# Kernel tuning notes

Hardware: AMD Instinct MI355X
Metric: run time of the kernel (lower is better)

## Reference

```python
import jax, jax.numpy as jnp
import numpy as np

D_MODEL = 1024
NUM_HEADS = 16


def setup_inputs() -> dict:
    key = jax.random.key(0)
    ks = jax.random.split(key, 11)
    B, S, D = 2, 2048, D_MODEL
    s = 1.0 / np.sqrt(D)
    return {
        "queries": jax.random.normal(ks[0], (B, S, D), jnp.float32),
        "keys": jax.random.normal(ks[1], (B, S, D), jnp.float32),
        "values": jax.random.normal(ks[2], (B, S, D), jnp.float32),
        "W_q": jax.random.normal(ks[3], (D, D), jnp.float32) * s,
        "b_q": jnp.zeros((D,), jnp.float32),
        "W_k": jax.random.normal(ks[4], (D, D), jnp.float32) * s,
        "b_k": jnp.zeros((D,), jnp.float32),
        "W_v": jax.random.normal(ks[5], (D, D), jnp.float32) * s,
        "b_v": jnp.zeros((D,), jnp.float32),
        "W_o": jax.random.normal(ks[6], (D, D), jnp.float32) * s,
        "b_o": jnp.zeros((D,), jnp.float32),
    }


def _split_heads(x, num_heads):
    # [B, S, D] -> [B, H, S, d_h]
    B, S, D = x.shape
    return x.reshape(B, S, num_heads, D // num_heads).transpose(0, 2, 1, 3)


def reference(queries, keys, values, W_q, b_q, W_k, b_k, W_v, b_v, W_o, b_o):
    H = NUM_HEADS
    Q = _split_heads(queries @ W_q.T + b_q, H)  # [B,H,S,dh]
    K = _split_heads(keys @ W_k.T + b_k, H)
    V = _split_heads(values @ W_v.T + b_v, H)
    d = Q.shape[-1]
    scores = jnp.einsum("bhqd,bhkd->bhqk", Q, K) / jnp.sqrt(jnp.asarray(d, Q.dtype))
    attn = jax.nn.softmax(scores, axis=-1)
    out = jnp.einsum("bhqk,bhkd->bhqd", attn, V)  # [B,H,S,dh]
    B, _, S, _ = out.shape
    out = out.transpose(0, 2, 1, 3).reshape(B, S, -1)  # combine heads
    return out @ W_o.T + b_o
```

## Files before the change

### kernel.cpp

```cpp
#include <hip/hip_runtime.h>
#include <cstdint>
#include <cmath>

typedef short s16x8 __attribute__((ext_vector_type(8)));
typedef short s16x4 __attribute__((ext_vector_type(4)));
typedef float f32x4 __attribute__((ext_vector_type(4)));
typedef unsigned int u32;

#define AS_G __attribute__((address_space(1)))
#define AS_L __attribute__((address_space(3)))

#define QSCALE 0.18033688011112042f

__device__ __forceinline__ void ld16_to_lds(const void* g, const void* l) {
    __builtin_amdgcn_global_load_lds((AS_G void*)(g), (AS_L void*)(l), 16, 0, 0);
}

__device__ __forceinline__ short f2bf(float f) {
    union { float f; uint32_t u; } v; v.f = f;
    uint32_t r = v.u + 0x7fffu + ((v.u >> 16) & 1u);
    return (short)(r >> 16);
}

template<int F32OUT, int NJ, int QKV>
__global__ __launch_bounds__(256, 3)
void gemm_bt(const short* __restrict__ Abase, long Az,
             const short* __restrict__ Wbase, long Wz,
             const float* __restrict__ bias0, const float* __restrict__ bias1,
             const float* __restrict__ bias2,
             void* __restrict__ Obase, long Oz,
             const int M, const int N, const int K)
{
    constexpr int BN = NJ * 32;
    constexpr int BSt = (BN * 4) / 256;
    constexpr int LPS = 2 + BSt;
    __shared__ __align__(16) short As[3][128 * 32];
    __shared__ __align__(16) short Bs[3][BN * 32];

    const int t = threadIdx.x, lane = t & 63, wv = t >> 6;
    const int wr = wv >> 1, wc = wv & 1;
    const int q4 = lane >> 4, l16 = lane & 15;

    const u32 gx = gridDim.x, gy = gridDim.y;
    u32 lin = blockIdx.x + gx * (blockIdx.y + gy * blockIdx.z);
    const u32 nwg = gx * gy * gridDim.z;
    if ((nwg & 7u) == 0u) lin = (lin & 7u) * (nwg >> 3) + (lin >> 3);
    const int bxs = lin % gx;
    const u32 rem = lin / gx;
    const int bys = rem % gy;
    const int z   = rem / gy;

    const short* A  = Abase + (long)z * Az;
    const short* Bt = Wbase + (long)z * Wz;
    const float* bias = (z == 0) ? bias0 : ((z == 1) ? bias1 : bias2);
    const float bmul = (QKV && z == 0) ? QSCALE : 1.0f;
    const int bn0 = bxs * BN, bm0 = bys * 128;

    f32x4 acc[4][NJ] = {};

    const short* gA[2];
    const short* gB[BSt];
    #pragma unroll
    for (int s = 0; s < 2; ++s) {
        const int c = t + 256 * s;
        const int r = c >> 2, g = (c & 3) ^ ((c >> 3) & 3);
        gA[s] = A + (size_t)(bm0 + r) * K + g * 8;
    }
    #pragma unroll
    for (int s = 0; s < BSt; ++s) {
        const int c = t + 256 * s;
        const int r = c >> 2, g = (c & 3) ^ ((c >> 3) & 3);
        gB[s] = Bt + (size_t)(bn0 + r) * K + g * 8;
    }

    auto stage = [&](int buf) {
        #pragma unroll
        for (int s = 0; s < 2; ++s) {
            ld16_to_lds(gA[s], &As[buf][(wv * 64 + 256 * s) * 8]);
            gA[s] += 32;
        }
        #pragma unroll
        for (int s = 0; s < BSt; ++s) {
            ld16_to_lds(gB[s], &Bs[buf][(wv * 64 + 256 * s) * 8]);
            gB[s] += 32;
        }
    };

    const int kIters = K >> 5;
    stage(0);
    stage(1);
    for (int kt = 0; kt < kIters; ++kt) {
        const int cur = kt % 3;
        if (kt < kIters - 1)
            asm volatile("s_waitcnt vmcnt(%0)" :: "n"(LPS) : "memory");
        else
            asm volatile("s_waitcnt vmcnt(0)" ::: "memory");
        __builtin_amdgcn_s_barrier();
        __builtin_amdgcn_sched_barrier(0);
        if (kt + 2 < kIters) stage((kt + 2) % 3);

        s16x8 aF[4], bF[NJ];
        #pragma unroll
        for (int i = 0; i < 4; ++i) {
            const int m = wr * 64 + i * 16 + l16;
            aF[i] = *(const s16x8*)&As[cur][m * 32 + (q4 ^ ((m >> 1) & 3)) * 8];
        }
        #pragma unroll
        for (int j = 0; j < NJ; ++j) {
            const int n = wc * (BN / 2) + j * 16 + l16;
            bF[j] = *(const s16x8*)&Bs[cur][n * 32 + (q4 ^ ((n >> 1) & 3)) * 8];
        }
        #pragma unroll
        for (int i = 0; i < 4; ++i)
            #pragma unroll
            for (int j = 0; j < NJ; ++j)
                acc[i][j] = __builtin_amdgcn_mfma_f32_16x16x32_bf16(
                    aF[i], bF[j], acc[i][j], 0, 0, 0);
    }

    #pragma unroll
    for (int j = 0; j < NJ; ++j) {
        const int col = bn0 + wc * (BN / 2) + j * 16 + l16;
        const float bj = bias[col] * bmul;
        #pragma unroll
        for (int i = 0; i < 4; ++i) {
            const int row0 = bm0 + wr * 64 + i * 16 + q4 * 4;
            if (QKV && z == 2) {
                s16x4 ov;
                #pragma unroll
                for (int r = 0; r < 4; ++r) ov[r] = f2bf(acc[i][j][r] + bj);
                *(s16x4*)(((short*)Obase + (long)z * Oz) +
                          (size_t)col * 4096 + row0) = ov;
            } else {
                #pragma unroll
                for (int r = 0; r < 4; ++r) {
                    const float v = acc[i][j][r] + bj;
                    if (F32OUT)
                        ((float*)Obase + (long)z * Oz)[(size_t)(row0 + r) * N + col] = v;
                    else
                        ((short*)Obase + (long)z * Oz)[(size_t)(row0 + r) * N + col] = f2bf(v);
                }
            }
        }
    }
}

__global__ __launch_bounds__(256, 4)
void attn_fwd(const short* __restrict__ Qp, const short* __restrict__ Kp,
              const short* __restrict__ VpT, short* __restrict__ Out)
{
    constexpr int D = 1024, S = 2048;
    __shared__ __align__(16) short Ks[2][512 * 8];
    __shared__ __align__(16) short Vt[2][512 * 8];

    const int t = threadIdx.x, lane = t & 63, wv = t >> 6;
    const int q4 = lane >> 4, l16 = lane & 15;
    const int bid = blockIdx.x;
    const int qt = (bid >> 3) & 31;
    const int hb = (bid & 7) * 4 + (bid >> 8);
    const int h = hb >> 1, b = hb & 1;
    const size_t rowB = (size_t)b * S;
    const int cb = h * 64;
    const int qrow0 = qt * 64 + wv * 16;

    s16x8 qF[2];
    #pragma unroll
    for (int tk = 0; tk < 2; ++tk)
        qF[tk] = *(const s16x8*)
            &Qp[(rowB + qrow0 + l16) * D + cb + tk * 32 + q4 * 8];

    f32x4 oacc[4] = {};
    f32x4 lacc = {};
    s16x8 onesF;
    #pragma unroll
    for (int e = 0; e < 8; ++e) onesF[e] = (short)0x3F80;

    const short* KpB = Kp + rowB * D + cb;
    const short* VtG = VpT + (size_t)cb * 4096 + b * 2048;

    auto stageKV = [&](int buf, int kv0) {
        #pragma unroll
        for (int s = 0; s < 2; ++s) {
            const int slot = (4 * s + wv) * 64 + lane;
            const int r = slot >> 3;
            const int kcs = (slot & 7) ^ (r & 7);
            ld16_to_lds(KpB + (size_t)(kv0 + r) * D + kcs * 8,
                        &Ks[buf][(wv * 64 + 256 * s) * 8]);
        }
        #pragma unroll
        for (int s = 0; s < 2; ++s) {
            const int c = t + 256 * s;
            const int d = c >> 3, kcp = c & 7;
            ld16_to_lds(VtG + (size_t)d * 4096 + kv0 + ((kcp ^ (d & 7)) * 8),
                        &Vt[buf][(wv * 64 + 256 * s) * 8]);
        }
    };

    stageKV(0, 0);

    for (int kvt = 0; kvt < 32; ++kvt) {
        const int kv0 = kvt * 64;
        __syncthreads();
        if (kvt < 31) stageKV((kvt + 1) & 1, kv0 + 64);

        f32x4 acc[4] = {};
        #pragma unroll
        for (int tk = 0; tk < 2; ++tk) {
            s16x8 kA[4];
            #pragma unroll
            for (int j = 0; j < 4; ++j)
                kA[j] = *(const s16x8*)
                    &Ks[kvt & 1][((j * 16 + l16) * 8 +
                                  ((tk * 4 + q4) ^ (l16 & 7))) * 8];
            #pragma unroll
            for (int j = 0; j < 4; ++j)
                acc[j] = __builtin_amdgcn_mfma_f32_16x16x32_bf16(
                    kA[j], qF[tk], acc[j], 0, 0, 0);
        }

        u32 c[4][2];
        #pragma unroll
        for (int j = 0; j < 4; ++j) {
            const float p0 = __builtin_amdgcn_exp2f(acc[j][0]);
            const float p1 = __builtin_amdgcn_exp2f(acc[j][1]);
            const float p2 = __builtin_amdgcn_exp2f(acc[j][2]);
            const float p3 = __builtin_amdgcn_exp2f(acc[j][3]);
            asm("v_cvt_pk_bf16_f32 %0, %1, %2" : "=v"(c[j][0]) : "v"(p0), "v"(p1));
            asm("v_cvt_pk_bf16_f32 %0, %1, %2" : "=v"(c[j][1]) : "v"(p2), "v"(p3));
        }

        union { s16x8 v; u32 w[4]; } pA[2];
        #pragma unroll
        for (int tkp = 0; tkp < 2; ++tkp) {
            #pragma unroll
            for (int bb = 0; bb < 2; ++bb) {
                u32 x = c[2 * tkp][bb], y = c[2 * tkp + 1][bb];
                asm("v_permlane32_swap_b32 %0, %1" : "+v"(x), "+v"(y));
                asm("v_permlane16_swap_b32 %0, %1" : "+v"(x), "+v"(y));
                pA[tkp].w[bb] = x;
                pA[tkp].w[2 + bb] = y;
            }
        }

        #pragma unroll
        for (int tkp = 0; tkp < 2; ++tkp) {
            lacc = __builtin_amdgcn_mfma_f32_16x16x32_bf16(
                pA[tkp].v, onesF, lacc, 0, 0, 0);
            #pragma unroll
            for (int jd = 0; jd < 4; ++jd) {
                const int d = jd * 16 + l16;
                const s16x8 vF = *(const s16x8*)
                    &Vt[kvt & 1][(d * 8 + ((tkp * 4 + q4) ^ (d & 7))) * 8];
                oacc[jd] = __builtin_amdgcn_mfma_f32_16x16x32_bf16(
                    pA[tkp].v, vF, oacc[jd], 0, 0, 0);
            }
        }
    }

    #pragma unroll
    for (int r = 0; r < 4; ++r) {
        const float inv = 1.0f / lacc[r];
        const size_t row = rowB + qrow0 + q4 * 4 + r;
        #pragma unroll
        for (int jd = 0; jd < 4; ++jd)
            Out[row * D + cb + jd * 16 + l16] = f2bf(oacc[jd][r] * inv);
    }
}

__global__ __launch_bounds__(256)
void cast_all(const float* __restrict__ q, const float* __restrict__ k,
              const float* __restrict__ v, const float* __restrict__ wq,
              const float* __restrict__ wk, const float* __restrict__ wv,
              const float* __restrict__ wo, short* __restrict__ out)
{
    const size_t i = ((size_t)blockIdx.x * 256 + threadIdx.x) * 8;
    const float* src; size_t off;
    if      (i < 4194304)  { src = q;  off = i; }
    else if (i < 8388608)  { src = k;  off = i - 4194304; }
    else if (i < 12582912) { src = v;  off = i - 8388608; }
    else if (i < 13631488) { src = wq; off = i - 12582912; }
    else if (i < 14680064) { src = wk; off = i - 13631488; }
    else if (i < 15728640) { src = wv; off = i - 14680064; }
    else                   { src = wo; off = i - 15728640; }
    const float m = (i >= 12582912 && i < 13631488) ? QSCALE : 1.0f;
    const float4 a = *(const float4*)(src + off);
    const float4 c = *(const float4*)(src + off + 4);
    s16x8 o;
    o[0] = f2bf(a.x * m); o[1] = f2bf(a.y * m); o[2] = f2bf(a.z * m); o[3] = f2bf(a.w * m);
    o[4] = f2bf(c.x * m); o[5] = f2bf(c.y * m); o[6] = f2bf(c.z * m); o[7] = f2bf(c.w * m);
    *(s16x8*)(out + i) = o;
}

extern "C" void kernel_launch(void* const* d_in, const int* in_sizes, int n_in,
                              void* d_out, int out_size, void* d_ws, size_t ws_size,
                              hipStream_t stream)
{
    const float* q  = (const float*)d_in[0];
    const float* k  = (const float*)d_in[1];
    const float* v  = (const float*)d_in[2];
    const float* Wq = (const float*)d_in[3];
    const float* bq = (const float*)d_in[4];
    const float* Wk = (const float*)d_in[5];
    const float* bk = (const float*)d_in[6];
    const float* Wv = (const float*)d_in[7];
    const float* bv = (const float*)d_in[8];
    const float* Wo = (const float*)d_in[9];
    const float* bo = (const float*)d_in[10];

    short* ws = (short*)d_ws;
    const long MEL = 1048576;
    short* Aq  = ws;
    short* Wqb = ws + 12 * MEL;
    short* Wob = ws + 15 * MEL;
    short* Qp  = ws + 16 * MEL;
    short* Kp  = ws + 20 * MEL;
    short* VpT = ws + 24 * MEL;
    short* AO  = ws;

    cast_all<<<8192, 256, 0, stream>>>(q, k, v, Wq, Wk, Wv, Wo, ws);

    gemm_bt<0, 4, 1><<<dim3(8, 32, 3), 256, 0, stream>>>(
        Aq, 4 * MEL, Wqb, 1 * MEL, bq, bk, bv, Qp, 4 * MEL, 4096, 1024, 1024);

    attn_fwd<<<1024, 256, 0, stream>>>(Qp, Kp, VpT, AO);

    gemm_bt<1, 2, 0><<<dim3(16, 32, 1), 256, 0, stream>>>(
        AO, 0, Wob, 0, bo, bo, bo, d_out, 0, 4096, 1024, 1024);
}
```

Measured before the change: 218.0 us.

## Process two 16-row query tiles per wave to reuse K/V LDS fragments

Each wave in the attention kernel now handles 32 query rows (two 16-row tiles) instead of 16. Block size grows to 128 query rows and the grid halves to 512 blocks. Each K and V fragment read from LDS now feeds two MFMAs, which halves LDS reads and global K/V staging per query row. The cost is more registers per thread and lower occupancy (launch bounds drop from 4 to 2 blocks per CU). With 512 blocks on a 256-CU part there is only about two blocks per CU, so latency hiding may suffer.

```diff
diff --git a/kernel.cpp b/kernel.cpp
--- a/kernel.cpp
+++ b/kernel.cpp
@@ -145,7 +145,7 @@
     }
 }
 
-__global__ __launch_bounds__(256, 4)
+__global__ __launch_bounds__(256, 2)
 void attn_fwd(const short* __restrict__ Qp, const short* __restrict__ Kp,
               const short* __restrict__ VpT, short* __restrict__ Out)
 {
@@ -156,21 +156,23 @@
     const int t = threadIdx.x, lane = t & 63, wv = t >> 6;
     const int q4 = lane >> 4, l16 = lane & 15;
     const int bid = blockIdx.x;
-    const int qt = (bid >> 3) & 31;
-    const int hb = (bid & 7) * 4 + (bid >> 8);
+    const int qt = (bid >> 3) & 15;
+    const int hb = (bid & 7) * 4 + (bid >> 7);
     const int h = hb >> 1, b = hb & 1;
     const size_t rowB = (size_t)b * S;
     const int cb = h * 64;
-    const int qrow0 = qt * 64 + wv * 16;
-
-    s16x8 qF[2];
-    #pragma unroll
-    for (int tk = 0; tk < 2; ++tk)
-        qF[tk] = *(const s16x8*)
-            &Qp[(rowB + qrow0 + l16) * D + cb + tk * 32 + q4 * 8];
-
-    f32x4 oacc[4] = {};
-    f32x4 lacc = {};
+    const int qrow0 = qt * 128 + wv * 32;
+
+    s16x8 qF[2][2];
+    #pragma unroll
+    for (int i = 0; i < 2; ++i)
+        #pragma unroll
+        for (int tk = 0; tk < 2; ++tk)
+            qF[i][tk] = *(const s16x8*)
+                &Qp[(rowB + qrow0 + i * 16 + l16) * D + cb + tk * 32 + q4 * 8];
+
+    f32x4 oacc[2][4] = {};
+    f32x4 lacc[2] = {};
     s16x8 onesF;
     #pragma unroll
     for (int e = 0; e < 8; ++e) onesF[e] = (short)0x3F80;
@@ -203,7 +205,7 @@
         __syncthreads();
         if (kvt < 31) stageKV((kvt + 1) & 1, kv0 + 64);
 
-        f32x4 acc[4] = {};
+        f32x4 acc[2][4] = {};
         #pragma unroll
         for (int tk = 0; tk < 2; ++tk) {
             s16x8 kA[4];
@@ -213,58 +215,68 @@
                     &Ks[kvt & 1][((j * 16 + l16) * 8 +
                                   ((tk * 4 + q4) ^ (l16 & 7))) * 8];
             #pragma unroll
-            for (int j = 0; j < 4; ++j)
-                acc[j] = __builtin_amdgcn_mfma_f32_16x16x32_bf16(
-                    kA[j], qF[tk], acc[j], 0, 0, 0);
-        }
-
-        u32 c[4][2];
-        #pragma unroll
-        for (int j = 0; j < 4; ++j) {
-            const float p0 = __builtin_amdgcn_exp2f(acc[j][0]);
-            const float p1 = __builtin_amdgcn_exp2f(acc[j][1]);
-            const float p2 = __builtin_amdgcn_exp2f(acc[j][2]);
-            const float p3 = __builtin_amdgcn_exp2f(acc[j][3]);
-            asm("v_cvt_pk_bf16_f32 %0, %1, %2" : "=v"(c[j][0]) : "v"(p0), "v"(p1));
-            asm("v_cvt_pk_bf16_f32 %0, %1, %2" : "=v"(c[j][1]) : "v"(p2), "v"(p3));
-        }
-
-        union { s16x8 v; u32 w[4]; } pA[2];
+            for (int j = 0; j < 4; ++j) {
+                acc[0][j] = __builtin_amdgcn_mfma_f32_16x16x32_bf16(
+                    kA[j], qF[0][tk], acc[0][j], 0, 0, 0);
+                acc[1][j] = __builtin_amdgcn_mfma_f32_16x16x32_bf16(
+                    kA[j], qF[1][tk], acc[1][j], 0, 0, 0);
+            }
+        }
+
+        union { s16x8 v; u32 w[4]; } pA[2][2];
+        #pragma unroll
+        for (int i = 0; i < 2; ++i) {
+            u32 cc[4][2];
+            #pragma unroll
+            for (int j = 0; j < 4; ++j) {
+                const float p0 = __builtin_amdgcn_exp2f(acc[i][j][0]);
+                const float p1 = __builtin_amdgcn_exp2f(acc[i][j][1]);
+                const float p2 = __builtin_amdgcn_exp2f(acc[i][j][2]);
+                const float p3 = __builtin_amdgcn_exp2f(acc[i][j][3]);
+                asm("v_cvt_pk_bf16_f32 %0, %1, %2" : "=v"(cc[j][0]) : "v"(p0), "v"(p1));
+                asm("v_cvt_pk_bf16_f32 %0, %1, %2" : "=v"(cc[j][1]) : "v"(p2), "v"(p3));
+            }
+            #pragma unroll
+            for (int tkp = 0; tkp < 2; ++tkp)
+                #pragma unroll
+                for (int bb = 0; bb < 2; ++bb) {
+                    u32 x = cc[2 * tkp][bb], y = cc[2 * tkp + 1][bb];
+                    asm("v_permlane32_swap_b32 %0, %1" : "+v"(x), "+v"(y));
+                    asm("v_permlane16_swap_b32 %0, %1" : "+v"(x), "+v"(y));
+                    pA[i][tkp].w[bb] = x;
+                    pA[i][tkp].w[2 + bb] = y;
+                }
+        }
+
         #pragma unroll
         for (int tkp = 0; tkp < 2; ++tkp) {
-            #pragma unroll
-            for (int bb = 0; bb < 2; ++bb) {
-                u32 x = c[2 * tkp][bb], y = c[2 * tkp + 1][bb];
-                asm("v_permlane32_swap_b32 %0, %1" : "+v"(x), "+v"(y));
-                asm("v_permlane16_swap_b32 %0, %1" : "+v"(x), "+v"(y));
-                pA[tkp].w[bb] = x;
-                pA[tkp].w[2 + bb] = y;
-            }
-        }
-
-        #pragma unroll
-        for (int tkp = 0; tkp < 2; ++tkp) {
-            lacc = __builtin_amdgcn_mfma_f32_16x16x32_bf16(
-                pA[tkp].v, onesF, lacc, 0, 0, 0);
+            lacc[0] = __builtin_amdgcn_mfma_f32_16x16x32_bf16(
+                pA[0][tkp].v, onesF, lacc[0], 0, 0, 0);
+            lacc[1] = __builtin_amdgcn_mfma_f32_16x16x32_bf16(
+                pA[1][tkp].v, onesF, lacc[1], 0, 0, 0);
             #pragma unroll
             for (int jd = 0; jd < 4; ++jd) {
                 const int d = jd * 16 + l16;
                 const s16x8 vF = *(const s16x8*)
                     &Vt[kvt & 1][(d * 8 + ((tkp * 4 + q4) ^ (d & 7))) * 8];
-                oacc[jd] = __builtin_amdgcn_mfma_f32_16x16x32_bf16(
-                    pA[tkp].v, vF, oacc[jd], 0, 0, 0);
+                oacc[0][jd] = __builtin_amdgcn_mfma_f32_16x16x32_bf16(
+                    pA[0][tkp].v, vF, oacc[0][jd], 0, 0, 0);
+                oacc[1][jd] = __builtin_amdgcn_mfma_f32_16x16x32_bf16(
+                    pA[1][tkp].v, vF, oacc[1][jd], 0, 0, 0);
             }
         }
     }
 
     #pragma unroll
-    for (int r = 0; r < 4; ++r) {
-        const float inv = 1.0f / lacc[r];
-        const size_t row = rowB + qrow0 + q4 * 4 + r;
-        #pragma unroll
-        for (int jd = 0; jd < 4; ++jd)
-            Out[row * D + cb + jd * 16 + l16] = f2bf(oacc[jd][r] * inv);
-    }
+    for (int i = 0; i < 2; ++i)
+        #pragma unroll
+        for (int r = 0; r < 4; ++r) {
+            const float inv = 1.0f / lacc[i][r];
+            const size_t row = rowB + qrow0 + i * 16 + q4 * 4 + r;
+            #pragma unroll
+            for (int jd = 0; jd < 4; ++jd)
+                Out[row * D + cb + jd * 16 + l16] = f2bf(oacc[i][jd][r] * inv);
+        }
 }
 
 __global__ __launch_bounds__(256)
@@ -322,7 +334,7 @@
     gemm_bt<0, 4, 1><<<dim3(8, 32, 3), 256, 0, stream>>>(
         Aq, 4 * MEL, Wqb, 1 * MEL, bq, bk, bv, Qp, 4 * MEL, 4096, 1024, 1024);
 
-    attn_fwd<<<1024, 256, 0, stream>>>(Qp, Kp, VpT, AO);
+    attn_fwd<<<512, 256, 0, stream>>>(Qp, Kp, VpT, AO);
 
     gemm_bt<1, 2, 0><<<dim3(16, 32, 1), 256, 0, stream>>>(
         AO, 0, Wob, 0, bo, bo, bo, d_out, 0, 4096, 1024, 1024);
```

Result: no change. 214.2 us (-1.8%).
